# Kernel tuning notes

Measured on AMD Instinct MI355X. Metric: run time of the kernel, lower is better.

The kernel has to match this reference:

```python
import jax, jax.numpy as jnp
import numpy as np
from jax import lax

B, N, F_IN, T = 1024, 22, 32, 32
K = 3
CHEV = 64     # nb_chev_filter
TIMEF = 64    # nb_time_filter
LN_EPS = 1e-5


def setup_inputs() -> dict:
    key = jax.random.key(0)
    ks = jax.random.split(key, 19)
    rn = lambda k, shape, s=0.1: (jax.random.normal(k, shape, jnp.float32) * s)
    return {
        "x": rn(ks[0], (B, N, F_IN, T), 1.0),
        # Temporal_Attention_layer params
        "U1": rn(ks[1], (N,)),
        "U2": rn(ks[2], (F_IN, N)),
        "U3": rn(ks[3], (F_IN,)),
        "be": rn(ks[4], (1, T, T)),
        "Ve": rn(ks[5], (T, T)),
        # Spatial_Attention_layer params
        "W1": rn(ks[6], (T,)),
        "W2": rn(ks[7], (F_IN, T)),
        "W3": rn(ks[8], (F_IN,)),
        "bs": rn(ks[9], (1, N, N)),
        "Vs": rn(ks[10], (N, N)),
        # cheb_conv_withSAt params
        "Theta": rn(ks[11], (K, F_IN, CHEV)),
        "node_emb": rn(ks[12], (N, N), 1.0),
        # time conv (1x3, pad (0,1)) and residual conv (1x1)
        "tconv_w": rn(ks[13], (TIMEF, CHEV, 1, 3)),
        "tconv_b": rn(ks[14], (TIMEF,)),
        "rconv_w": rn(ks[15], (TIMEF, F_IN, 1, 1)),
        "rconv_b": rn(ks[16], (TIMEF,)),
        # LayerNorm over nb_time_filter
        "ln_g": jnp.ones((TIMEF,), jnp.float32),
        "ln_b": jnp.zeros((TIMEF,), jnp.float32),
    }


def reference(x, U1, U2, U3, be, Ve, W1, W2, W3, bs, Vs, Theta, node_emb,
              tconv_w, tconv_b, rconv_w, rconv_b, ln_g, ln_b):
    Bx, Nx, Fx, Tx = x.shape

    # ---- Temporal attention: E_normalized [B, T, T] ----
    # lhs = ((x.permute(0,3,2,1) @ U1) @ U2)  -> [B, T, N]
    lhs_t = jnp.einsum('bnft,n->btf', x, U1) @ U2          # [B,T,N]
    rhs_t = jnp.einsum('f,bnft->bnt', U3, x)               # [B,N,T]
    prod_t = jnp.einsum('btn,bns->bts', lhs_t, rhs_t)      # [B,T,T]
    E = jnp.einsum('ts,bsu->btu', Ve, jax.nn.sigmoid(prod_t + be))
    E_norm = jax.nn.softmax(E, axis=1)                     # softmax over dim=1

    # x_TAt = reshape(x, [B, N*F, T]) @ E_norm  -> [B, N, F, T]
    x_TAt = (x.reshape(Bx, Nx * Fx, Tx) @ E_norm).reshape(Bx, Nx, Fx, Tx)

    # ---- Spatial attention on x_TAt: S_normalized [B, N, N] ----
    lhs_s = jnp.einsum('bnft,t->bnf', x_TAt, W1) @ W2      # [B,N,T]
    rhs_s = jnp.einsum('f,bnft->bnt', W3, x_TAt)           # [B,N,T]
    prod_s = jnp.einsum('bnt,bmt->bnm', lhs_s, rhs_s)      # [B,N,N]
    S = jnp.einsum('nm,bml->bnl', Vs, jax.nn.sigmoid(prod_s + bs))
    S_norm = jax.nn.softmax(S, axis=1)                     # softmax over dim=1

    # ---- Chebyshev graph conv with adaptive supports (vectorized over T) ----
    supports = jax.nn.softmax(jax.nn.relu(node_emb @ node_emb.T), axis=1)
    support_set = [jnp.eye(Nx, dtype=x.dtype), supports]
    for _ in range(2, K):
        support_set.append(2.0 * supports @ support_set[-1] - support_set[-2])

    out = jnp.zeros((Bx, Nx, CHEV, Tx), x.dtype)
    for k in range(K):
        A_k = support_set[k][None, :, :] * S_norm          # [B,N,N]
        # rhs[b,m,f,t] = sum_n A_k[b,n,m] * x[b,n,f,t]  (A_k^T @ graph_signal)
        rhs = jnp.einsum('bnm,bnft->bmft', A_k, x)
        out = out + jnp.einsum('bmft,fo->bmot', rhs, Theta[k])
    spatial_gcn = jax.nn.relu(out)                         # [B,N,CHEV,T]

    # ---- Temporal conv (1x3, pad (0,1)) on [B, CHEV, N, T] ----
    dn = ('NCHW', 'OIHW', 'NCHW')
    t_in = spatial_gcn.transpose(0, 2, 1, 3)               # [B,CHEV,N,T]
    t_out = lax.conv_general_dilated(t_in, tconv_w, (1, 1), ((0, 0), (1, 1)),
                                     dimension_numbers=dn)
    t_out = t_out + tconv_b[None, :, None, None]           # [B,TIMEF,N,T]

    # ---- Residual conv (1x1) on [B, F_in, N, T] ----
    r_in = x.transpose(0, 2, 1, 3)
    r_out = lax.conv_general_dilated(r_in, rconv_w, (1, 1), ((0, 0), (0, 0)),
                                     dimension_numbers=dn)
    r_out = r_out + rconv_b[None, :, None, None]           # [B,TIMEF,N,T]

    # ---- Residual add, ReLU, LayerNorm over channel dim ----
    y = jax.nn.relu(r_out + t_out).transpose(0, 3, 2, 1)   # [B,T,N,TIMEF]
    mu = jnp.mean(y, axis=-1, keepdims=True)
    var = jnp.var(y, axis=-1, keepdims=True)
    y = (y - mu) * lax.rsqrt(var + LN_EPS) * ln_g + ln_b
    return y.transpose(0, 2, 3, 1)                         # [B,N,TIMEF,T]
```

## Files before the change

kernel.cpp:

```cpp
#include <hip/hip_runtime.h>
#include <math.h>


typedef unsigned short u16;
typedef __attribute__((ext_vector_type(8))) short short8;
typedef __attribute__((ext_vector_type(4))) float f32x4;

__device__ __forceinline__ float sigm(float v){ return 1.f/(1.f+expf(-v)); }

__device__ __forceinline__ u16 f2bf(float x){
  union { float f; unsigned u; } c; c.f = x;
  unsigned r = (c.u + 0x7fffu + ((c.u>>16)&1u)) >> 16;
  return (u16)r;
}

__global__ void k_supports(const float* __restrict__ emb, float* __restrict__ wsT){
  __shared__ float M[484];
  __shared__ float T1s[484];
  int tid = threadIdx.x;
  if (tid < 484){
    int n = tid/22, m = tid - (tid/22)*22;
    float s = 0.f;
    for (int j=0;j<22;j++) s += emb[n*22+j]*emb[m*22+j];
    M[tid] = fmaxf(s, 0.f);
  }
  __syncthreads();
  if (tid < 22){
    float mx = -1e30f;
    for (int m=0;m<22;m++) mx = fmaxf(mx, M[tid*22+m]);
    float s = 0.f;
    for (int m=0;m<22;m++) s += expf(M[tid*22+m]-mx);
    float inv = 1.f/s;
    for (int m=0;m<22;m++) T1s[tid*22+m] = expf(M[tid*22+m]-mx)*inv;
  }
  __syncthreads();
  if (tid < 484){
    int n = tid/22, m = tid - (tid/22)*22;
    float s = 0.f;
    for (int p=0;p<22;p++) s += T1s[n*22+p]*T1s[p*22+m];
    wsT[tid]      = T1s[tid];
    wsT[484+tid]  = 2.f*s - ((n==m)?1.f:0.f);
  }
}

__global__ void k_prep(const float* __restrict__ Theta,
                       const float* __restrict__ tw, const float* __restrict__ tb,
                       const float* __restrict__ rw, const float* __restrict__ rb,
                       u16* __restrict__ thA, u16* __restrict__ wA, float* __restrict__ wsB){
  int tid = blockIdx.x*256 + threadIdx.x;
  if (tid < 6144){
    int j = tid&7, l = (tid>>3)&63, blk = tid>>9;
    int ks = blk>>2, ci = blk&3, r = l&15, g = l>>4;
    int kf = 32*ks + 8*g + j, c = 16*ci + r;
    thA[tid] = f2bf(Theta[kf*64 + c]);
  } else if (tid < 20480){
    int e = tid - 6144;
    int j = e&7, l = (e>>3)&63, blk = e>>9;
    int ks = blk>>2, oi = blk&3, r = l&15, g = l>>4;
    int k = 32*ks + 8*g + j, o = 16*oi + r;
    float v = (k < 192) ? tw[o*192 + (k&63)*3 + (k>>6)] : rw[o*32 + (k-192)];
    wA[e] = f2bf(v);
  } else if (tid < 20544){
    int o = tid - 20480; wsB[o] = tb[o] + rb[o];
  }
}

__global__ __launch_bounds__(512) void k_attn(
    const float* __restrict__ x,
    const float* __restrict__ U1, const float* __restrict__ U2, const float* __restrict__ U3,
    const float* __restrict__ be, const float* __restrict__ Ve,
    const float* __restrict__ W1, const float* __restrict__ W2, const float* __restrict__ W3,
    const float* __restrict__ bs, const float* __restrict__ Vs,
    float* __restrict__ snorm){
  int b = blockIdx.x, tid = threadIdx.x;
  const float* xb = x + (size_t)b*22528;
  __shared__ float xu1[1024];
  __shared__ float rhs_t[704];
  __shared__ float lhs_t[704];
  __shared__ float sigp[1024];
  __shared__ float Em[1024];
  __shared__ float sm[1024];
  __shared__ float w1e[32];
  __shared__ float xw3[704];
  __shared__ float lhsS[704];
  __shared__ float lhs2[704];
  __shared__ float rhsS[704];
  __shared__ float sig2[484];
  __shared__ float Sl[484];

  for (int idx=tid; idx<1024; idx+=512){
    float a=0.f;
    for (int n=0;n<22;n++) a = fmaf(xb[n*1024 + idx], U1[n], a);
    xu1[idx]=a;
  }
  for (int idx=tid; idx<704; idx+=512){
    int n = idx>>5, t = idx&31; float a=0.f, c=0.f;
    for (int f=0;f<32;f++){ float xv = xb[n*1024+f*32+t]; a = fmaf(U3[f],xv,a); c = fmaf(W3[f],xv,c); }
    rhs_t[idx]=a; xw3[idx]=c;
  }
  __syncthreads();
  for (int idx=tid; idx<704; idx+=512){
    int t = idx/22, n2 = idx - t*22; float a=0.f;
    for (int f=0;f<32;f++) a = fmaf(xu1[f*32+t], U2[f*22+n2], a);
    lhs_t[idx]=a;
  }
  __syncthreads();
  for (int idx=tid; idx<1024; idx+=512){
    int s = idx>>5, u = idx&31; float p=0.f;
    for (int n=0;n<22;n++) p = fmaf(lhs_t[s*22+n], rhs_t[n*32+u], p);
    sigp[idx] = sigm(p + be[idx]);
  }
  __syncthreads();
  for (int idx=tid; idx<1024; idx+=512){
    int t = idx>>5, u = idx&31; float a=0.f;
    for (int s2=0;s2<32;s2++) a = fmaf(Ve[t*32+s2], sigp[s2*32+u], a);
    Em[idx]=a;
  }
  __syncthreads();
  if (tid<32){
    int u=tid; float mx=-1e30f;
    for (int t=0;t<32;t++) mx = fmaxf(mx, Em[t*32+u]);
    float s=0.f; for (int t=0;t<32;t++) s += expf(Em[t*32+u]-mx);
    float inv = 1.f/s;
    for (int t=0;t<32;t++) sm[t*32+u] = expf(Em[t*32+u]-mx)*inv;
  }
  __syncthreads();
  if (tid<32){ float a=0.f; for (int t2=0;t2<32;t2++) a = fmaf(sm[tid*32+t2], W1[t2], a); w1e[tid]=a; }
  __syncthreads();
  for (int idx=tid; idx<704; idx+=512){
    int n = idx>>5, f = idx&31; float a=0.f;
    for (int u=0;u<32;u++) a = fmaf(xb[n*1024+f*32+u], w1e[u], a);
    lhsS[idx]=a;
  }
  __syncthreads();
  for (int idx=tid; idx<704; idx+=512){
    int n = idx>>5, t = idx&31; float a=0.f;
    for (int f=0;f<32;f++) a = fmaf(lhsS[n*32+f], W2[f*32+t], a);
    lhs2[idx]=a;
  }
  for (int idx=tid; idx<704; idx+=512){
    int mm = idx>>5, t = idx&31; float a=0.f;
    for (int u=0;u<32;u++) a = fmaf(xw3[mm*32+u], sm[u*32+t], a);
    rhsS[idx]=a;
  }
  __syncthreads();
  for (int idx=tid; idx<484; idx+=512){
    int a_ = idx/22, l = idx - (idx/22)*22; float p=0.f;
    for (int t=0;t<32;t++) p = fmaf(lhs2[a_*32+t], rhsS[l*32+t], p);
    sig2[idx] = sigm(p + bs[idx]);
  }
  __syncthreads();
  for (int idx=tid; idx<484; idx+=512){
    int n = idx/22, l = idx - (idx/22)*22; float s=0.f;
    for (int mm=0;mm<22;mm++) s = fmaf(Vs[n*22+mm], sig2[mm*22+l], s);
    Sl[idx]=s;
  }
  __syncthreads();
  if (tid<22){
    int l=tid; float mx=-1e30f;
    for (int n=0;n<22;n++) mx = fmaxf(mx, Sl[n*22+l]);
    float s=0.f; for (int n=0;n<22;n++) s += expf(Sl[n*22+l]-mx);
    float inv=1.f/s;
    for (int n=0;n<22;n++) snorm[(size_t)b*484 + n*22 + l] = expf(Sl[n*22+l]-mx)*inv;
  }
}

__device__ __forceinline__ void fma4(float4& a, float c, const float4& v){
  a.x = fmaf(c, v.x, a.x); a.y = fmaf(c, v.y, a.y);
  a.z = fmaf(c, v.z, a.z); a.w = fmaf(c, v.w, a.w);
}

__global__ __launch_bounds__(256, 6) void k_fused(
    const float* __restrict__ x,
    const float* __restrict__ wsT, const float* __restrict__ snorm,
    const u16* __restrict__ thA, const u16* __restrict__ wA, const float* __restrict__ wsB,
    const float* __restrict__ lng, const float* __restrict__ lnb,
    float* __restrict__ out){
  __shared__ __align__(16) u16 GtU[2][32*72];
  __shared__ __align__(16) u16 sgTU[2][34*72];
  __shared__ __align__(16) u16 xTU[2][32*40];
  __shared__ __align__(16) float akL[2][2][22];
  __shared__ float smm[2];

  int wg = blockIdx.x;
  int logical = (wg & 7)*1408 + (wg >> 3);
  int b = logical/11, mp = logical - b*11;
  int m0 = mp*2;
  int tid = threadIdx.x;
  const float* xb = x + (size_t)b*22528;

  if (tid < 128){
    int mi = tid>>6, r6 = tid&63;
    int row = (r6>>5) ? 33 : 0, c2 = r6&31;
    *(unsigned*)&sgTU[mi][row*72 + c2*2] = 0u;
  }
  if (tid < 88){
    int mi = tid/44, rem = tid - mi*44;
    int k1 = rem/22, n = rem - k1*22;
    int m = m0 + mi;
    akL[mi][k1][n] = wsT[k1*484 + n*22 + m] * snorm[(size_t)b*484 + n*22 + m];
  }
  if (tid < 2) smm[tid] = snorm[(size_t)b*484 + (m0+tid)*23];
  __syncthreads();

  {
    float4 acc[2][2];
    #pragma unroll
    for (int a=0;a<2;a++){ acc[a][0]=float4{0,0,0,0}; acc[a][1]=float4{0,0,0,0}; }
    const float4* x4 = (const float4*)xb;
    #pragma unroll 2
    for (int n=0;n<22;n++){
      float4 xv = x4[n*256 + tid];
      fma4(acc[0][0], akL[0][0][n], xv);
      fma4(acc[0][1], akL[0][1][n], xv);
      fma4(acc[1][0], akL[1][0][n], xv);
      fma4(acc[1][1], akL[1][1][n], xv);
    }
    int f = tid>>3, t0 = (tid&7)*4;
    #pragma unroll
    for (int mi=0;mi<2;mi++){
      float4 xm = x4[(m0+mi)*256 + tid];
      u16* xd = &xTU[mi][0];
      xd[(t0+0)*40 + f] = f2bf(xm.x);
      xd[(t0+1)*40 + f] = f2bf(xm.y);
      xd[(t0+2)*40 + f] = f2bf(xm.z);
      xd[(t0+3)*40 + f] = f2bf(xm.w);
      #pragma unroll
      for (int k1=0;k1<2;k1++){
        float4 v = acc[mi][k1];
        u16* gd = &GtU[mi][k1*32 + f];
        gd[(t0+0)*72] = f2bf(v.x);
        gd[(t0+1)*72] = f2bf(v.y);
        gd[(t0+2)*72] = f2bf(v.z);
        gd[(t0+3)*72] = f2bf(v.w);
      }
    }
  }
  __syncthreads();

  int w = tid>>6, l = tid&63, r = l&15, g = l>>4;

  {
    const u16* tA = thA + (size_t)(w*64 + l)*8;
    short8 a0 = *(const short8*)(tA);
    short8 a1 = *(const short8*)(tA + 2048);
    short8 a2 = *(const short8*)(tA + 4096);
    #pragma unroll
    for (int mi=0;mi<2;mi++){
      float sm_ = smm[mi];
      #pragma unroll
      for (int ti=0; ti<2; ++ti){
        f32x4 a12 = {0.f,0.f,0.f,0.f}, ax = {0.f,0.f,0.f,0.f};
        const u16* gp = &GtU[mi][(ti*16 + r)*72 + 8*g];
        a12 = __builtin_amdgcn_mfma_f32_16x16x32_bf16(a1, *(const short8*)(gp),      a12, 0,0,0);
        a12 = __builtin_amdgcn_mfma_f32_16x16x32_bf16(a2, *(const short8*)(gp + 32), a12, 0,0,0);
        const u16* xp = &xTU[mi][(ti*16 + r)*40 + 8*g];
        ax  = __builtin_amdgcn_mfma_f32_16x16x32_bf16(a0, *(const short8*)(xp),      ax,  0,0,0);
        int row = 1 + ti*16 + r, c0 = w*16 + g*4;
        float v0 = fmaxf(fmaf(sm_, ax[0], a12[0]), 0.f);
        float v1 = fmaxf(fmaf(sm_, ax[1], a12[1]), 0.f);
        float v2 = fmaxf(fmaf(sm_, ax[2], a12[2]), 0.f);
        float v3 = fmaxf(fmaf(sm_, ax[3], a12[3]), 0.f);
        unsigned u01 = (unsigned)f2bf(v0) | ((unsigned)f2bf(v1)<<16);
        unsigned u23 = (unsigned)f2bf(v2) | ((unsigned)f2bf(v3)<<16);
        *(unsigned*)&sgTU[mi][row*72 + c0]     = u01;
        *(unsigned*)&sgTU[mi][row*72 + c0 + 2] = u23;
      }
    }
  }
  __syncthreads();

  f32x4 acc[2][2];
  acc[0][0]=f32x4{0,0,0,0}; acc[0][1]=f32x4{0,0,0,0};
  acc[1][0]=f32x4{0,0,0,0}; acc[1][1]=f32x4{0,0,0,0};
  {
    const u16* pA = wA + (size_t)(w*64 + l)*8;
    #pragma unroll
    for (int ks=0; ks<6; ++ks){
      short8 wk = *(const short8*)(pA + ks*2048);
      int seg = ks>>1, colb = (ks&1)*32 + 8*g;
      #pragma unroll
      for (int mi=0;mi<2;mi++){
        const u16* q0 = &sgTU[mi][(r + seg)*72 + colb];
        acc[mi][0] = __builtin_amdgcn_mfma_f32_16x16x32_bf16(wk, *(const short8*)(q0),         acc[mi][0], 0,0,0);
        acc[mi][1] = __builtin_amdgcn_mfma_f32_16x16x32_bf16(wk, *(const short8*)(q0 + 16*72), acc[mi][1], 0,0,0);
      }
    }
    short8 wk = *(const short8*)(pA + 6*2048);
    #pragma unroll
    for (int mi=0;mi<2;mi++){
      const u16* q = &xTU[mi][r*40 + 8*g];
      acc[mi][0] = __builtin_amdgcn_mfma_f32_16x16x32_bf16(wk, *(const short8*)(q),         acc[mi][0], 0,0,0);
      acc[mi][1] = __builtin_amdgcn_mfma_f32_16x16x32_bf16(wk, *(const short8*)(q + 16*40), acc[mi][1], 0,0,0);
    }
  }

  float4 bias4 = ((const float4*)wsB)[w*4 + g];
  float bb[4] = {bias4.x, bias4.y, bias4.z, bias4.w};
  float y[2][2][4];
  float s1[2][2] = {{0.f,0.f},{0.f,0.f}}, s2[2][2] = {{0.f,0.f},{0.f,0.f}};
  #pragma unroll
  for (int mi=0;mi<2;mi++){
    #pragma unroll
    for (int h=0;h<2;h++){
      #pragma unroll
      for (int i=0;i<4;i++){
        float v = fmaxf(acc[mi][h][i] + bb[i], 0.f);
        y[mi][h][i] = v;
        s1[mi][h] += v;
        s2[mi][h] = fmaf(v, v, s2[mi][h]);
      }
      s1[mi][h] += __shfl_xor(s1[mi][h],16); s1[mi][h] += __shfl_xor(s1[mi][h],32);
      s2[mi][h] += __shfl_xor(s2[mi][h],16); s2[mi][h] += __shfl_xor(s2[mi][h],32);
    }
  }
  float* p1 = (float*)&GtU[0][0];
  float* p2 = p1 + 256;
  if (l < 16){
    #pragma unroll
    for (int mi=0;mi<2;mi++){
      p1[(mi*32 + l)*4 + w]      = s1[mi][0];
      p1[(mi*32 + 16 + l)*4 + w] = s1[mi][1];
      p2[(mi*32 + l)*4 + w]      = s2[mi][0];
      p2[(mi*32 + 16 + l)*4 + w] = s2[mi][1];
    }
  }
  __syncthreads();
  float4 g4 = ((const float4*)lng)[w*4 + g];
  float4 b4 = ((const float4*)lnb)[w*4 + g];
  float gg[4]={g4.x,g4.y,g4.z,g4.w}, bgg[4]={b4.x,b4.y,b4.z,b4.w};
  #pragma unroll
  for (int mi=0;mi<2;mi++){
    float4 q1a = ((const float4*)p1)[mi*32 + r],      q2a = ((const float4*)p2)[mi*32 + r];
    float4 q1b = ((const float4*)p1)[mi*32 + 16 + r], q2b = ((const float4*)p2)[mi*32 + 16 + r];
    float S1a = q1a.x+q1a.y+q1a.z+q1a.w, S2a = q2a.x+q2a.y+q2a.z+q2a.w;
    float S1b = q1b.x+q1b.y+q1b.z+q1b.w, S2b = q2b.x+q2b.y+q2b.z+q2b.w;
    float mu0 = S1a*(1.f/64.f), var0 = S2a*(1.f/64.f) - mu0*mu0, rs0 = rsqrtf(var0 + 1e-5f);
    float mu1 = S1b*(1.f/64.f), var1 = S2b*(1.f/64.f) - mu1*mu1, rs1 = rsqrtf(var1 + 1e-5f);
    float* ob = out + ((size_t)(b*22 + m0 + mi)*64 + (w*16 + g*4))*32;
    #pragma unroll
    for (int i=0;i<4;i++){
      ob[i*32 + r]      = (y[mi][0][i]-mu0)*rs0*gg[i] + bgg[i];
      ob[i*32 + 16 + r] = (y[mi][1][i]-mu1)*rs1*gg[i] + bgg[i];
    }
  }
}

extern "C" void kernel_launch(void* const* d_in, const int* in_sizes, int n_in,
                              void* d_out, int out_size, void* d_ws, size_t ws_size,
                              hipStream_t stream){
  const float* x     = (const float*)d_in[0];
  const float* U1    = (const float*)d_in[1];
  const float* U2    = (const float*)d_in[2];
  const float* U3    = (const float*)d_in[3];
  const float* be    = (const float*)d_in[4];
  const float* Ve    = (const float*)d_in[5];
  const float* W1    = (const float*)d_in[6];
  const float* W2    = (const float*)d_in[7];
  const float* W3    = (const float*)d_in[8];
  const float* bs    = (const float*)d_in[9];
  const float* Vs    = (const float*)d_in[10];
  const float* Theta = (const float*)d_in[11];
  const float* emb   = (const float*)d_in[12];
  const float* tw    = (const float*)d_in[13];
  const float* tb    = (const float*)d_in[14];
  const float* rw    = (const float*)d_in[15];
  const float* rb    = (const float*)d_in[16];
  const float* lng   = (const float*)d_in[17];
  const float* lnb   = (const float*)d_in[18];
  float* out = (float*)d_out;
  float* wsf = (float*)d_ws;
  float* wsT   = wsf;
  float* snorm = wsf + 1024;
  u16*   thA   = (u16*)(wsf + 496640);
  u16*   wA    = (u16*)(wsf + 499712);
  float* wsB   = wsf + 506880;

  k_supports<<<1, 512, 0, stream>>>(emb, wsT);
  k_prep<<<81, 256, 0, stream>>>(Theta, tw, tb, rw, rb, thA, wA, wsB);
  k_attn<<<1024, 512, 0, stream>>>(x, U1,U2,U3, be,Ve, W1,W2,W3, bs,Vs, snorm);
  k_fused<<<1024*11, 256, 0, stream>>>(x, wsT, snorm, thA, wA, wsB, lng, lnb, out);
}
```

Baseline: 160.6 us.

## Merge setup kernels, parallelize attention softmaxes with shuffles, use packed FMA

Merges the supports and weight-prep kernels into one launch to save a kernel launch. Rewrites the temporal and spatial softmaxes in the attention kernel, plus the W1 reduction, as wave-parallel __shfl_xor reductions instead of loops run serially by 32 or 22 threads. Changes the diffusion accumulation in the fused kernel to float2 elementwise FMAs so the compiler can emit packed FMA instructions. The shuffle softmaxes assume tid>>4 covers all 32 columns in a 512-thread block, and the bit-exact reduction order differs from before.

```diff
diff --git a/kernel.cpp b/kernel.cpp
--- a/kernel.cpp
+++ b/kernel.cpp
@@ -5,6 +5,7 @@
 typedef unsigned short u16;
 typedef __attribute__((ext_vector_type(8))) short short8;
 typedef __attribute__((ext_vector_type(4))) float f32x4;
+typedef __attribute__((ext_vector_type(2))) float f32x2;
 
 __device__ __forceinline__ float sigm(float v){ return 1.f/(1.f+expf(-v)); }
 
@@ -14,15 +15,38 @@
   return (u16)r;
 }
 
-__global__ void k_supports(const float* __restrict__ emb, float* __restrict__ wsT){
+__global__ void k_sup_prep(const float* __restrict__ emb, float* __restrict__ wsT,
+                           const float* __restrict__ Theta,
+                           const float* __restrict__ tw, const float* __restrict__ tb,
+                           const float* __restrict__ rw, const float* __restrict__ rb,
+                           u16* __restrict__ thA, u16* __restrict__ wA, float* __restrict__ wsB){
+  if (blockIdx.x < 81){
+    int tid = blockIdx.x*256 + threadIdx.x;
+    if (tid < 6144){
+      int j = tid&7, l = (tid>>3)&63, blk = tid>>9;
+      int ks = blk>>2, ci = blk&3, r = l&15, g = l>>4;
+      int kf = 32*ks + 8*g + j, c = 16*ci + r;
+      thA[tid] = f2bf(Theta[kf*64 + c]);
+    } else if (tid < 20480){
+      int e = tid - 6144;
+      int j = e&7, l = (e>>3)&63, blk = e>>9;
+      int ks = blk>>2, oi = blk&3, r = l&15, g = l>>4;
+      int k = 32*ks + 8*g + j, o = 16*oi + r;
+      float v = (k < 192) ? tw[o*192 + (k&63)*3 + (k>>6)] : rw[o*32 + (k-192)];
+      wA[e] = f2bf(v);
+    } else if (tid < 20544){
+      int o = tid - 20480; wsB[o] = tb[o] + rb[o];
+    }
+    return;
+  }
   __shared__ float M[484];
   __shared__ float T1s[484];
   int tid = threadIdx.x;
-  if (tid < 484){
-    int n = tid/22, m = tid - (tid/22)*22;
+  for (int idx=tid; idx<484; idx+=256){
+    int n = idx/22, m = idx - (idx/22)*22;
     float s = 0.f;
     for (int j=0;j<22;j++) s += emb[n*22+j]*emb[m*22+j];
-    M[tid] = fmaxf(s, 0.f);
+    M[idx] = fmaxf(s, 0.f);
   }
   __syncthreads();
   if (tid < 22){
@@ -34,34 +58,12 @@
     for (int m=0;m<22;m++) T1s[tid*22+m] = expf(M[tid*22+m]-mx)*inv;
   }
   __syncthreads();
-  if (tid < 484){
-    int n = tid/22, m = tid - (tid/22)*22;
+  for (int idx=tid; idx<484; idx+=256){
+    int n = idx/22, m = idx - (idx/22)*22;
     float s = 0.f;
     for (int p=0;p<22;p++) s += T1s[n*22+p]*T1s[p*22+m];
-    wsT[tid]      = T1s[tid];
-    wsT[484+tid]  = 2.f*s - ((n==m)?1.f:0.f);
-  }
-}
-
-__global__ void k_prep(const float* __restrict__ Theta,
-                       const float* __restrict__ tw, const float* __restrict__ tb,
-                       const float* __restrict__ rw, const float* __restrict__ rb,
-                       u16* __restrict__ thA, u16* __restrict__ wA, float* __restrict__ wsB){
-  int tid = blockIdx.x*256 + threadIdx.x;
-  if (tid < 6144){
-    int j = tid&7, l = (tid>>3)&63, blk = tid>>9;
-    int ks = blk>>2, ci = blk&3, r = l&15, g = l>>4;
-    int kf = 32*ks + 8*g + j, c = 16*ci + r;
-    thA[tid] = f2bf(Theta[kf*64 + c]);
-  } else if (tid < 20480){
-    int e = tid - 6144;
-    int j = e&7, l = (e>>3)&63, blk = e>>9;
-    int ks = blk>>2, oi = blk&3, r = l&15, g = l>>4;
-    int k = 32*ks + 8*g + j, o = 16*oi + r;
-    float v = (k < 192) ? tw[o*192 + (k&63)*3 + (k>>6)] : rw[o*32 + (k-192)];
-    wA[e] = f2bf(v);
-  } else if (tid < 20544){
-    int o = tid - 20480; wsB[o] = tb[o] + rb[o];
+    wsT[idx]      = T1s[idx];
+    wsT[484+idx]  = 2.f*s - ((n==m)?1.f:0.f);
   }
 }
 
@@ -117,15 +119,28 @@
     Em[idx]=a;
   }
   __syncthreads();
-  if (tid<32){
-    int u=tid; float mx=-1e30f;
-    for (int t=0;t<32;t++) mx = fmaxf(mx, Em[t*32+u]);
-    float s=0.f; for (int t=0;t<32;t++) s += expf(Em[t*32+u]-mx);
+  {
+    int u = tid>>4, th = tid&15;
+    float e0 = Em[(2*th)*32 + u], e1 = Em[(2*th+1)*32 + u];
+    float mx = fmaxf(e0, e1);
+    #pragma unroll
+    for (int mask=1; mask<16; mask<<=1) mx = fmaxf(mx, __shfl_xor(mx, mask));
+    float x0 = expf(e0-mx), x1 = expf(e1-mx);
+    float s = x0 + x1;
+    #pragma unroll
+    for (int mask=1; mask<16; mask<<=1) s += __shfl_xor(s, mask);
     float inv = 1.f/s;
-    for (int t=0;t<32;t++) sm[t*32+u] = expf(Em[t*32+u]-mx)*inv;
-  }
-  __syncthreads();
-  if (tid<32){ float a=0.f; for (int t2=0;t2<32;t2++) a = fmaf(sm[tid*32+t2], W1[t2], a); w1e[tid]=a; }
+    sm[(2*th)*32 + u]   = x0*inv;
+    sm[(2*th+1)*32 + u] = x1*inv;
+  }
+  __syncthreads();
+  {
+    int u = tid>>4, th = tid&15;
+    float pw = fmaf(sm[u*32 + 2*th], W1[2*th], sm[u*32 + 2*th+1]*W1[2*th+1]);
+    #pragma unroll
+    for (int mask=1; mask<16; mask<<=1) pw += __shfl_xor(pw, mask);
+    if (th==0) w1e[u] = pw;
+  }
   __syncthreads();
   for (int idx=tid; idx<704; idx+=512){
     int n = idx>>5, f = idx&31; float a=0.f;
@@ -156,18 +171,20 @@
     Sl[idx]=s;
   }
   __syncthreads();
-  if (tid<22){
-    int l=tid; float mx=-1e30f;
-    for (int n=0;n<22;n++) mx = fmaxf(mx, Sl[n*22+l]);
-    float s=0.f; for (int n=0;n<22;n++) s += expf(Sl[n*22+l]-mx);
-    float inv=1.f/s;
-    for (int n=0;n<22;n++) snorm[(size_t)b*484 + n*22 + l] = expf(Sl[n*22+l]-mx)*inv;
-  }
-}
-
-__device__ __forceinline__ void fma4(float4& a, float c, const float4& v){
-  a.x = fmaf(c, v.x, a.x); a.y = fmaf(c, v.y, a.y);
-  a.z = fmaf(c, v.z, a.z); a.w = fmaf(c, v.w, a.w);
+  {
+    int grp = tid>>5, nn = tid&31;
+    for (int l = grp; l < 22; l += 16){
+      float v = (nn<22) ? Sl[nn*22 + l] : -1e30f;
+      float mx = v;
+      #pragma unroll
+      for (int mask=1; mask<32; mask<<=1) mx = fmaxf(mx, __shfl_xor(mx, mask));
+      float e = (nn<22) ? expf(v-mx) : 0.f;
+      float s = e;
+      #pragma unroll
+      for (int mask=1; mask<32; mask<<=1) s += __shfl_xor(s, mask);
+      if (nn<22) snorm[(size_t)b*484 + nn*22 + l] = e/s;
+    }
+  }
 }
 
 __global__ __launch_bounds__(256, 6) void k_fused(
@@ -204,22 +221,31 @@
   __syncthreads();
 
   {
-    float4 acc[2][2];
-    #pragma unroll
-    for (int a=0;a<2;a++){ acc[a][0]=float4{0,0,0,0}; acc[a][1]=float4{0,0,0,0}; }
+    f32x2 acc[2][2][2];
+    #pragma unroll
+    for (int a=0;a<2;a++)
+      #pragma unroll
+      for (int k1=0;k1<2;k1++){ acc[a][k1][0]=f32x2{0,0}; acc[a][k1][1]=f32x2{0,0}; }
     const float4* x4 = (const float4*)xb;
     #pragma unroll 2
     for (int n=0;n<22;n++){
       float4 xv = x4[n*256 + tid];
-      fma4(acc[0][0], akL[0][0][n], xv);
-      fma4(acc[0][1], akL[0][1][n], xv);
-      fma4(acc[1][0], akL[1][0][n], xv);
-      fma4(acc[1][1], akL[1][1][n], xv);
+      f32x2 xlo = {xv.x, xv.y}, xhi = {xv.z, xv.w};
+      #pragma unroll
+      for (int mi=0;mi<2;mi++){
+        #pragma unroll
+        for (int k1=0;k1<2;k1++){
+          float a = akL[mi][k1][n];
+          f32x2 av = {a, a};
+          acc[mi][k1][0] = __builtin_elementwise_fma(av, xlo, acc[mi][k1][0]);
+          acc[mi][k1][1] = __builtin_elementwise_fma(av, xhi, acc[mi][k1][1]);
+        }
+      }
     }
     int f = tid>>3, t0 = (tid&7)*4;
     #pragma unroll
     for (int mi=0;mi<2;mi++){
-      float4 xm = x4[(m0+mi)*256 + tid];
+      float4 xm = ((const float4*)xb)[(m0+mi)*256 + tid];
       u16* xd = &xTU[mi][0];
       xd[(t0+0)*40 + f] = f2bf(xm.x);
       xd[(t0+1)*40 + f] = f2bf(xm.y);
@@ -227,12 +253,11 @@
       xd[(t0+3)*40 + f] = f2bf(xm.w);
       #pragma unroll
       for (int k1=0;k1<2;k1++){
-        float4 v = acc[mi][k1];
         u16* gd = &GtU[mi][k1*32 + f];
-        gd[(t0+0)*72] = f2bf(v.x);
-        gd[(t0+1)*72] = f2bf(v.y);
-        gd[(t0+2)*72] = f2bf(v.z);
-        gd[(t0+3)*72] = f2bf(v.w);
+        gd[(t0+0)*72] = f2bf(acc[mi][k1][0][0]);
+        gd[(t0+1)*72] = f2bf(acc[mi][k1][0][1]);
+        gd[(t0+2)*72] = f2bf(acc[mi][k1][1][0]);
+        gd[(t0+3)*72] = f2bf(acc[mi][k1][1][1]);
       }
     }
   }
@@ -376,8 +401,7 @@
   u16*   wA    = (u16*)(wsf + 499712);
   float* wsB   = wsf + 506880;
 
-  k_supports<<<1, 512, 0, stream>>>(emb, wsT);
-  k_prep<<<81, 256, 0, stream>>>(Theta, tw, tb, rw, rb, thA, wA, wsB);
+  k_sup_prep<<<82, 256, 0, stream>>>(emb, wsT, Theta, tw, tb, rw, rb, thA, wA, wsB);
   k_attn<<<1024, 512, 0, stream>>>(x, U1,U2,U3, be,Ve, W1,W2,W3, bs,Vs, snorm);
   k_fused<<<1024*11, 256, 0, stream>>>(x, wsT, snorm, thA, wA, wsB, lng, lnb, out);
 }
```

Result: faster. 155.4 us (-3.3%).
